# Optimization experiments

Measured on AMD Instinct MI355X. Metric: run time of the kernel, lower is better.

Reference implementation:

```python
import jax, jax.numpy as jnp
import numpy as np

N = 50000      # nodes
E = 800000     # edges (avg degree 16)
IN = 128       # in_channels
OUT = 64       # out_channels
K = 2          # propagation hops


def setup_inputs() -> dict:
    key = jax.random.key(0)
    k1, k2, k3 = jax.random.split(key, 3)
    x = jax.random.normal(k1, (N, IN), dtype=jnp.float32)
    edge_index = jax.random.randint(k2, (2, E), 0, N, dtype=jnp.int32)
    # SGConv's internal Linear(in, out): weight [OUT, IN], bias [OUT]
    W = jax.random.normal(k3, (OUT, IN), dtype=jnp.float32) / np.sqrt(IN)
    b = jnp.zeros((OUT,), dtype=jnp.float32)
    return {"x": x, "edge_index": edge_index, "W": W, "b": b}


def reference(x, edge_index, W, b):
    # GCN normalization with self-loops (PyG gcn_norm, add_self_loops=True)
    row, col = edge_index[0], edge_index[1]
    loops = jnp.arange(N, dtype=edge_index.dtype)
    row = jnp.concatenate([row, loops])   # source nodes
    col = jnp.concatenate([col, loops])   # target nodes
    ones = jnp.ones((E + N,), dtype=x.dtype)
    deg = jax.ops.segment_sum(ones, col, num_segments=N)          # in-degree incl. self-loop
    deg_inv_sqrt = jnp.where(deg > 0, jax.lax.rsqrt(deg), 0.0)
    norm = deg_inv_sqrt[row] * deg_inv_sqrt[col]                  # [E+N]

    # K-hop propagation: x <- D^{-1/2} (A+I) D^{-1/2} x
    for _ in range(K):
        x = jax.ops.segment_sum(x[row] * norm[:, None], col, num_segments=N)

    # final linear; dropout is identity in eval mode (training=False)
    return x @ W.T + b
```

## Files before the change

### kernel.cpp

```cpp
#include <hip/hip_runtime.h>
#include <hip/hip_bf16.h>
#include <hip/hip_fp16.h>

#define IN_CH 128
#define OUT_CH 64
#define NB 512

typedef _Float16 hh2 __attribute__((ext_vector_type(2)));

__global__ void __launch_bounds__(512) histo_kernel(const int* __restrict__ col,
                                                    int* __restrict__ blkcnt,
                                                    int E, int chunk) {
    __shared__ int h[256];
    int blk = blockIdx.x, tid = threadIdx.x;
    if (tid < 256) h[tid] = 0;
    __syncthreads();
    int s = blk * chunk, e = min(s + chunk, E);
    for (int i = s + tid; i < e; i += 512)
        atomicAdd(&h[col[i] >> 8], 1);
    __syncthreads();
    if (tid < 256) blkcnt[blk * 256 + tid] = h[tid];
}

__global__ void __launch_bounds__(256) scanblk_kernel(int* __restrict__ blkcnt,
                                                      int* __restrict__ totals) {
    __shared__ int ps[256];
    int b = blockIdx.x, tid = threadIdx.x;
    int i0 = (2 * tid) * 256 + b, i1 = (2 * tid + 1) * 256 + b;
    int a0 = blkcnt[i0], a1 = blkcnt[i1];
    int lsum = a0 + a1;
    ps[tid] = lsum;
    __syncthreads();
    for (int d = 1; d < 256; d <<= 1) {
        int t = 0;
        if (tid >= d) t = ps[tid - d];
        __syncthreads();
        if (tid >= d) ps[tid] += t;
        __syncthreads();
    }
    int excl = ps[tid] - lsum;
    blkcnt[i0] = excl;
    blkcnt[i1] = excl + a0;
    if (tid == 255) totals[b] = excl + lsum;
}

__global__ void __launch_bounds__(512) bucket_scatter_kernel(const int* __restrict__ row,
                                                             const int* __restrict__ col,
                                                             const int* __restrict__ blkcnt,
                                                             const int* __restrict__ totals,
                                                             unsigned int* __restrict__ tmp,
                                                             int E, int chunk, int nbkt) {
    __shared__ int ps[256];
    __shared__ int cur[256];
    int blk = blockIdx.x, tid = threadIdx.x;
    int v = 0;
    if (tid < 256) { v = (tid < nbkt) ? totals[tid] : 0; ps[tid] = v; }
    __syncthreads();
    for (int d = 1; d < 256; d <<= 1) {
        int t = 0;
        if (tid < 256 && tid >= d) t = ps[tid - d];
        __syncthreads();
        if (tid < 256 && tid >= d) ps[tid] += t;
        __syncthreads();
    }
    if (tid < 256) cur[tid] = (ps[tid] - v) + blkcnt[blk * 256 + tid];
    __syncthreads();
    int s = blk * chunk, e = min(s + chunk, E);
    for (int i = s + tid; i < e; i += 512) {
        int c = col[i], r = row[i];
        int p = atomicAdd(&cur[c >> 8], 1);
        tmp[p] = ((unsigned)(c & 255) << 16) | (unsigned)r;
    }
}

__global__ void __launch_bounds__(512) bucket_sort_kernel(const unsigned int* __restrict__ tmp,
                                                          const int* __restrict__ totals,
                                                          int* __restrict__ off,
                                                          float* __restrict__ dis,
                                                          unsigned short* __restrict__ eidx,
                                                          int nbkt, int E, int n) {
    __shared__ int bs[256];
    __shared__ int cntl[256];
    __shared__ int sc[256];
    __shared__ int posl[256];
    int b = blockIdx.x, tid = threadIdx.x;
    int v = 0;
    if (tid < 256) { v = (tid < nbkt) ? totals[tid] : 0; bs[tid] = v; }
    __syncthreads();
    for (int d = 1; d < 256; d <<= 1) {
        int t = 0;
        if (tid < 256 && tid >= d) t = bs[tid - d];
        __syncthreads();
        if (tid < 256 && tid >= d) bs[tid] += t;
        __syncthreads();
    }
    if (tid < 256) bs[tid] -= v;
    if (tid < 256) cntl[tid] = 0;
    __syncthreads();
    int s = bs[b];
    int e = s + ((b < nbkt) ? totals[b] : 0);
    for (int i = s + tid; i < e; i += 512)
        atomicAdd(&cntl[tmp[i] >> 16], 1);
    __syncthreads();
    int c = 0;
    if (tid < 256) { c = cntl[tid]; sc[tid] = c; }
    __syncthreads();
    for (int d = 1; d < 256; d <<= 1) {
        int t = 0;
        if (tid < 256 && tid >= d) t = sc[tid - d];
        __syncthreads();
        if (tid < 256 && tid >= d) sc[tid] += t;
        __syncthreads();
    }
    if (tid < 256) {
        int excl = sc[tid] - c;
        int gid = (b << 8) + tid;
        if (gid < n) {
            off[gid] = s + excl;
            dis[gid] = rsqrtf((float)(c + 1));
        }
        posl[tid] = s + excl;
    }
    if (b == 0 && tid == 0) off[n] = E;
    __syncthreads();
    for (int i = s + tid; i < e; i += 512) {
        unsigned int w = tmp[i];
        int p = atomicAdd(&posl[w >> 16], 1);
        eidx[p] = (unsigned short)(w & 0xFFFFu);
    }
}

__global__ void __launch_bounds__(256) gemm_kernel(const float* __restrict__ x,
                                                   const float* __restrict__ W,
                                                   const float* __restrict__ dis,
                                                   __half* __restrict__ z, int n) {
    __shared__ hh2 Xs[64 * 66];
    __shared__ hh2 Ws[64 * 66];
    int t = threadIdx.x;
    int m0 = blockIdx.x * 64;
#pragma unroll
    for (int r = 0; r < 8; ++r) {
        int f = t + 256 * r;
        int o = f >> 5, kq = f & 31;
        float4 w = ((const float4*)W)[f];
        Ws[o * 66 + kq * 2]     = hh2{(_Float16)w.x, (_Float16)w.y};
        Ws[o * 66 + kq * 2 + 1] = hh2{(_Float16)w.z, (_Float16)w.w};
    }
#pragma unroll
    for (int r = 0; r < 8; ++r) {
        int f = t + 256 * r;
        int node = f >> 5, kq = f & 31;
        int gv = min(m0 + node, n - 1);
        float4 xv = ((const float4*)(x + (size_t)gv * IN_CH))[kq];
        Xs[node * 66 + kq * 2]     = hh2{(_Float16)xv.x, (_Float16)xv.y};
        Xs[node * 66 + kq * 2 + 1] = hh2{(_Float16)xv.z, (_Float16)xv.w};
    }
    __syncthreads();
    int tx = t & 15, ty = t >> 4;
    float acc[4][4];
#pragma unroll
    for (int i = 0; i < 4; ++i)
#pragma unroll
        for (int j = 0; j < 4; ++j) acc[i][j] = 0.f;

#pragma unroll 4
    for (int kq = 0; kq < 32; ++kq) {
        hh2 xa0[4], xa1[4], wb0[4], wb1[4];
#pragma unroll
        for (int i = 0; i < 4; ++i) {
            int base = (tx + 16 * i) * 66 + kq * 2;
            xa0[i] = Xs[base]; xa1[i] = Xs[base + 1];
        }
#pragma unroll
        for (int j = 0; j < 4; ++j) {
            int base = (ty * 4 + j) * 66 + kq * 2;
            wb0[j] = Ws[base]; wb1[j] = Ws[base + 1];
        }
#pragma unroll
        for (int i = 0; i < 4; ++i)
#pragma unroll
            for (int j = 0; j < 4; ++j) {
                float s = acc[i][j];
                s = __builtin_amdgcn_fdot2(xa0[i], wb0[j], s, false);
                s = __builtin_amdgcn_fdot2(xa1[i], wb1[j], s, false);
                acc[i][j] = s;
            }
    }
#pragma unroll
    for (int i = 0; i < 4; ++i) {
        int v = m0 + tx + 16 * i;
        if (v < n) {
            float dv = dis[v];
            union { __half2 h[2]; float2 f; } u;
            u.h[0] = __floats2half2_rn(dv * acc[i][0], dv * acc[i][1]);
            u.h[1] = __floats2half2_rn(dv * acc[i][2], dv * acc[i][3]);
            *(float2*)&z[(size_t)v * OUT_CH + ty * 4] = u.f;
        }
    }
}

#define ACC8(raw) { const __half2* h2_ = (const __half2*)&(raw);              \
    float2 f0_ = __half22float2(h2_[0]), f1_ = __half22float2(h2_[1]);        \
    float2 f2_ = __half22float2(h2_[2]), f3_ = __half22float2(h2_[3]);        \
    a0 += f0_.x; a1 += f0_.y; a2 += f1_.x; a3 += f1_.y;                       \
    a4 += f2_.x; a5 += f2_.y; a6 += f3_.x; a7 += f3_.y; }

template <int MODE>
__global__ void __launch_bounds__(256) hop_kernel(const __half* __restrict__ zin,
                                                  void* __restrict__ out,
                                                  const unsigned short* __restrict__ eidx,
                                                  const int* __restrict__ off,
                                                  const float* __restrict__ dis,
                                                  const float* __restrict__ bias, int n) {
    int v = (int)((blockIdx.x * 256 + threadIdx.x) >> 6);
    if (v >= n) return;
    int lane = threadIdx.x & 63;
    int grp = lane >> 3;
    int sub = lane & 7;
    int s = off[v], e = off[v + 1];
    float dv = dis[v];
    float a0 = 0.f, a1 = 0.f, a2 = 0.f, a3 = 0.f;
    float a4 = 0.f, a5 = 0.f, a6 = 0.f, a7 = 0.f;
    if (grp == 0) {
        float4 raw = ((const float4*)(zin + (size_t)v * OUT_CH))[sub];
        ACC8(raw);
    }
    int i0 = s + grp;
    int i1 = i0 + 8, i2 = i0 + 16, i3 = i0 + 24;
    bool h0 = i0 < e, h1 = i1 < e, h2 = i2 < e, h3 = i3 < e;
    int r0 = h0 ? (int)eidx[i0] : 0;
    int r1 = h1 ? (int)eidx[i1] : 0;
    int r2 = h2 ? (int)eidx[i2] : 0;
    int r3 = h3 ? (int)eidx[i3] : 0;
    float4 rA = make_float4(0.f, 0.f, 0.f, 0.f);
    float4 rB = make_float4(0.f, 0.f, 0.f, 0.f);
    float4 rC = make_float4(0.f, 0.f, 0.f, 0.f);
    float4 rD = make_float4(0.f, 0.f, 0.f, 0.f);
    if (h0) rA = ((const float4*)(zin + (size_t)r0 * OUT_CH))[sub];
    if (h1) rB = ((const float4*)(zin + (size_t)r1 * OUT_CH))[sub];
    if (h2) rC = ((const float4*)(zin + (size_t)r2 * OUT_CH))[sub];
    if (h3) rD = ((const float4*)(zin + (size_t)r3 * OUT_CH))[sub];
    ACC8(rA); ACC8(rB); ACC8(rC); ACC8(rD);
    if (e - s > 32) {
        int j0 = s + 32 + grp, j1 = j0 + 8;
        bool g0 = j0 < e, g1 = j1 < e;
        int q0 = g0 ? (int)eidx[j0] : 0;
        int q1 = g1 ? (int)eidx[j1] : 0;
        while (g0) {
            int k0 = j0 + 16, k1 = j1 + 16;
            bool f0 = k0 < e, f1 = k1 < e;
            int p0 = f0 ? (int)eidx[k0] : 0;
            int p1 = f1 ? (int)eidx[k1] : 0;
            float4 xA = make_float4(0.f, 0.f, 0.f, 0.f);
            float4 xB = make_float4(0.f, 0.f, 0.f, 0.f);
            if (g0) xA = ((const float4*)(zin + (size_t)q0 * OUT_CH))[sub];
            if (g1) xB = ((const float4*)(zin + (size_t)q1 * OUT_CH))[sub];
            ACC8(xA); ACC8(xB);
            j0 = k0; j1 = k1; q0 = p0; q1 = p1; g0 = f0; g1 = f1;
        }
    }
#pragma unroll
    for (int m = 8; m <= 32; m <<= 1) {
        a0 += __shfl_xor(a0, m, 64); a1 += __shfl_xor(a1, m, 64);
        a2 += __shfl_xor(a2, m, 64); a3 += __shfl_xor(a3, m, 64);
        a4 += __shfl_xor(a4, m, 64); a5 += __shfl_xor(a5, m, 64);
        a6 += __shfl_xor(a6, m, 64); a7 += __shfl_xor(a7, m, 64);
    }
    if (grp == 0) {
        if (MODE == 0) {
            float sc = dv * dv;
            union { __half2 h[4]; float4 f; } u;
            u.h[0] = __floats2half2_rn(sc * a0, sc * a1);
            u.h[1] = __floats2half2_rn(sc * a2, sc * a3);
            u.h[2] = __floats2half2_rn(sc * a4, sc * a5);
            u.h[3] = __floats2half2_rn(sc * a6, sc * a7);
            ((float4*)((__half*)out + (size_t)v * OUT_CH))[sub] = u.f;
        } else {
            const float4* bp = (const float4*)(bias + sub * 8);
            float4 b0 = bp[0], b1 = bp[1];
            float* op = (float*)out + (size_t)v * OUT_CH + sub * 8;
            *(float4*)op = make_float4(fmaf(dv, a0, b0.x), fmaf(dv, a1, b0.y),
                                       fmaf(dv, a2, b0.z), fmaf(dv, a3, b0.w));
            *(float4*)(op + 4) = make_float4(fmaf(dv, a4, b1.x), fmaf(dv, a5, b1.y),
                                             fmaf(dv, a6, b1.z), fmaf(dv, a7, b1.w));
        }
    }
}

extern "C" void kernel_launch(void* const* d_in, const int* in_sizes, int n_in,
                              void* d_out, int out_size, void* d_ws, size_t ws_size,
                              hipStream_t stream) {
    const float* x = (const float*)d_in[0];
    const int* ei = (const int*)d_in[1];
    const float* W = (const float*)d_in[2];
    const float* b = (const float*)d_in[3];
    int n = in_sizes[0] / IN_CH;
    int E = in_sizes[1] / 2;
    const int* row = ei;
    const int* col = ei + E;

    char* ws = (char*)d_ws;
    size_t o = 0;
    auto alloc = [&](size_t bytes) -> void* {
        void* p = ws + o;
        o += (bytes + 255) & ~(size_t)255;
        return p;
    };
    int nbkt = (n + 255) >> 8;
    int chunk = (E + NB - 1) / NB;

    int*            blkcnt = (int*)alloc((size_t)NB * 256 * 4);
    int*            totals = (int*)alloc(256 * 4);
    unsigned int*   tmp    = (unsigned int*)alloc((size_t)E * 4);
    int*            off    = (int*)alloc((size_t)(n + 1) * 4);
    float*          dis    = (float*)alloc((size_t)n * 4);
    unsigned short* eidx   = (unsigned short*)alloc((size_t)E * 2);
    __half*         zA     = (__half*)alloc((size_t)n * OUT_CH * 2);
    __half*         zB     = (__half*)alloc((size_t)n * OUT_CH * 2);

    histo_kernel<<<NB, 512, 0, stream>>>(col, blkcnt, E, chunk);
    scanblk_kernel<<<nbkt, 256, 0, stream>>>(blkcnt, totals);
    bucket_scatter_kernel<<<NB, 512, 0, stream>>>(row, col, blkcnt, totals, tmp, E, chunk, nbkt);
    bucket_sort_kernel<<<nbkt, 512, 0, stream>>>(tmp, totals, off, dis, eidx, nbkt, E, n);
    gemm_kernel<<<(n + 63) / 64, 256, 0, stream>>>(x, W, dis, zA, n);
    int hopBlocks = (n + 3) / 4;
    hop_kernel<0><<<hopBlocks, 256, 0, stream>>>(zA, zB, eidx, off, dis, nullptr, n);
    hop_kernel<1><<<hopBlocks, 256, 0, stream>>>(zB, d_out, eidx, off, dis, b, n);
}
```

Before: 157.6 us.

## Merge preprocessing and compute stages into two cooperative persistent kernels

Replaces seven separate kernel launches with two cooperative kernels that separate the former stages with grid-wide syncs. One kernel covers histogram, scan, bucket scatter and bucket sort. The other runs the GEMM and both propagation hops with grid-stride loops. The aim is to cut per-launch overhead and inter-kernel gaps, at the cost of grid.sync latency and fewer resident blocks for the hop phases. The original multi-kernel path is kept as a fallback if the cooperative launch fails.

```diff
diff --git a/kernel.cpp b/kernel.cpp
--- a/kernel.cpp
+++ b/kernel.cpp
@@ -1,200 +1,132 @@
 #include <hip/hip_runtime.h>
+#include <hip/hip_cooperative_groups.h>
 #include <hip/hip_bf16.h>
 #include <hip/hip_fp16.h>
+
+namespace cg = cooperative_groups;
 
 #define IN_CH 128
 #define OUT_CH 64
 #define NB 512
+#define CB 1024
 
 typedef _Float16 hh2 __attribute__((ext_vector_type(2)));
 
-__global__ void __launch_bounds__(512) histo_kernel(const int* __restrict__ col,
-                                                    int* __restrict__ blkcnt,
-                                                    int E, int chunk) {
-    __shared__ int h[256];
+__global__ void __launch_bounds__(512, 4) pre_kernel(
+    const int* __restrict__ row, const int* __restrict__ col,
+    int* __restrict__ blkcnt, int* __restrict__ totals,
+    unsigned int* __restrict__ tmp, int* __restrict__ off,
+    float* __restrict__ dis, unsigned short* __restrict__ eidx,
+    int E, int n, int chunk, int nbkt)
+{
+    __shared__ int sm[1024];
+    cg::grid_group grid = cg::this_grid();
     int blk = blockIdx.x, tid = threadIdx.x;
-    if (tid < 256) h[tid] = 0;
-    __syncthreads();
-    int s = blk * chunk, e = min(s + chunk, E);
-    for (int i = s + tid; i < e; i += 512)
-        atomicAdd(&h[col[i] >> 8], 1);
-    __syncthreads();
-    if (tid < 256) blkcnt[blk * 256 + tid] = h[tid];
-}
-
-__global__ void __launch_bounds__(256) scanblk_kernel(int* __restrict__ blkcnt,
-                                                      int* __restrict__ totals) {
-    __shared__ int ps[256];
-    int b = blockIdx.x, tid = threadIdx.x;
-    int i0 = (2 * tid) * 256 + b, i1 = (2 * tid + 1) * 256 + b;
-    int a0 = blkcnt[i0], a1 = blkcnt[i1];
-    int lsum = a0 + a1;
-    ps[tid] = lsum;
-    __syncthreads();
-    for (int d = 1; d < 256; d <<= 1) {
-        int t = 0;
-        if (tid >= d) t = ps[tid - d];
-        __syncthreads();
-        if (tid >= d) ps[tid] += t;
-        __syncthreads();
-    }
-    int excl = ps[tid] - lsum;
-    blkcnt[i0] = excl;
-    blkcnt[i1] = excl + a0;
-    if (tid == 255) totals[b] = excl + lsum;
-}
-
-__global__ void __launch_bounds__(512) bucket_scatter_kernel(const int* __restrict__ row,
-                                                             const int* __restrict__ col,
-                                                             const int* __restrict__ blkcnt,
-                                                             const int* __restrict__ totals,
-                                                             unsigned int* __restrict__ tmp,
-                                                             int E, int chunk, int nbkt) {
-    __shared__ int ps[256];
-    __shared__ int cur[256];
-    int blk = blockIdx.x, tid = threadIdx.x;
-    int v = 0;
-    if (tid < 256) { v = (tid < nbkt) ? totals[tid] : 0; ps[tid] = v; }
-    __syncthreads();
-    for (int d = 1; d < 256; d <<= 1) {
-        int t = 0;
-        if (tid < 256 && tid >= d) t = ps[tid - d];
-        __syncthreads();
-        if (tid < 256 && tid >= d) ps[tid] += t;
-        __syncthreads();
-    }
-    if (tid < 256) cur[tid] = (ps[tid] - v) + blkcnt[blk * 256 + tid];
-    __syncthreads();
-    int s = blk * chunk, e = min(s + chunk, E);
-    for (int i = s + tid; i < e; i += 512) {
-        int c = col[i], r = row[i];
-        int p = atomicAdd(&cur[c >> 8], 1);
-        tmp[p] = ((unsigned)(c & 255) << 16) | (unsigned)r;
-    }
-}
-
-__global__ void __launch_bounds__(512) bucket_sort_kernel(const unsigned int* __restrict__ tmp,
-                                                          const int* __restrict__ totals,
-                                                          int* __restrict__ off,
-                                                          float* __restrict__ dis,
-                                                          unsigned short* __restrict__ eidx,
-                                                          int nbkt, int E, int n) {
-    __shared__ int bs[256];
-    __shared__ int cntl[256];
-    __shared__ int sc[256];
-    __shared__ int posl[256];
-    int b = blockIdx.x, tid = threadIdx.x;
-    int v = 0;
-    if (tid < 256) { v = (tid < nbkt) ? totals[tid] : 0; bs[tid] = v; }
-    __syncthreads();
-    for (int d = 1; d < 256; d <<= 1) {
-        int t = 0;
-        if (tid < 256 && tid >= d) t = bs[tid - d];
-        __syncthreads();
-        if (tid < 256 && tid >= d) bs[tid] += t;
-        __syncthreads();
-    }
-    if (tid < 256) bs[tid] -= v;
-    if (tid < 256) cntl[tid] = 0;
-    __syncthreads();
-    int s = bs[b];
-    int e = s + ((b < nbkt) ? totals[b] : 0);
-    for (int i = s + tid; i < e; i += 512)
-        atomicAdd(&cntl[tmp[i] >> 16], 1);
-    __syncthreads();
-    int c = 0;
-    if (tid < 256) { c = cntl[tid]; sc[tid] = c; }
-    __syncthreads();
-    for (int d = 1; d < 256; d <<= 1) {
-        int t = 0;
-        if (tid < 256 && tid >= d) t = sc[tid - d];
-        __syncthreads();
-        if (tid < 256 && tid >= d) sc[tid] += t;
-        __syncthreads();
-    }
-    if (tid < 256) {
-        int excl = sc[tid] - c;
-        int gid = (b << 8) + tid;
-        if (gid < n) {
-            off[gid] = s + excl;
-            dis[gid] = rsqrtf((float)(c + 1));
-        }
-        posl[tid] = s + excl;
-    }
-    if (b == 0 && tid == 0) off[n] = E;
-    __syncthreads();
-    for (int i = s + tid; i < e; i += 512) {
-        unsigned int w = tmp[i];
-        int p = atomicAdd(&posl[w >> 16], 1);
-        eidx[p] = (unsigned short)(w & 0xFFFFu);
-    }
-}
-
-__global__ void __launch_bounds__(256) gemm_kernel(const float* __restrict__ x,
-                                                   const float* __restrict__ W,
-                                                   const float* __restrict__ dis,
-                                                   __half* __restrict__ z, int n) {
-    __shared__ hh2 Xs[64 * 66];
-    __shared__ hh2 Ws[64 * 66];
-    int t = threadIdx.x;
-    int m0 = blockIdx.x * 64;
-#pragma unroll
-    for (int r = 0; r < 8; ++r) {
-        int f = t + 256 * r;
-        int o = f >> 5, kq = f & 31;
-        float4 w = ((const float4*)W)[f];
-        Ws[o * 66 + kq * 2]     = hh2{(_Float16)w.x, (_Float16)w.y};
-        Ws[o * 66 + kq * 2 + 1] = hh2{(_Float16)w.z, (_Float16)w.w};
-    }
-#pragma unroll
-    for (int r = 0; r < 8; ++r) {
-        int f = t + 256 * r;
-        int node = f >> 5, kq = f & 31;
-        int gv = min(m0 + node, n - 1);
-        float4 xv = ((const float4*)(x + (size_t)gv * IN_CH))[kq];
-        Xs[node * 66 + kq * 2]     = hh2{(_Float16)xv.x, (_Float16)xv.y};
-        Xs[node * 66 + kq * 2 + 1] = hh2{(_Float16)xv.z, (_Float16)xv.w};
-    }
-    __syncthreads();
-    int tx = t & 15, ty = t >> 4;
-    float acc[4][4];
-#pragma unroll
-    for (int i = 0; i < 4; ++i)
-#pragma unroll
-        for (int j = 0; j < 4; ++j) acc[i][j] = 0.f;
-
-#pragma unroll 4
-    for (int kq = 0; kq < 32; ++kq) {
-        hh2 xa0[4], xa1[4], wb0[4], wb1[4];
-#pragma unroll
-        for (int i = 0; i < 4; ++i) {
-            int base = (tx + 16 * i) * 66 + kq * 2;
-            xa0[i] = Xs[base]; xa1[i] = Xs[base + 1];
-        }
-#pragma unroll
-        for (int j = 0; j < 4; ++j) {
-            int base = (ty * 4 + j) * 66 + kq * 2;
-            wb0[j] = Ws[base]; wb1[j] = Ws[base + 1];
-        }
-#pragma unroll
-        for (int i = 0; i < 4; ++i)
-#pragma unroll
-            for (int j = 0; j < 4; ++j) {
-                float s = acc[i][j];
-                s = __builtin_amdgcn_fdot2(xa0[i], wb0[j], s, false);
-                s = __builtin_amdgcn_fdot2(xa1[i], wb1[j], s, false);
-                acc[i][j] = s;
+
+    if (tid < 256) sm[tid] = 0;
+    __syncthreads();
+    {
+        int s = blk * chunk, e = min(s + chunk, E);
+        for (int i = s + tid; i < e; i += 512)
+            atomicAdd(&sm[col[i] >> 8], 1);
+    }
+    __syncthreads();
+    if (tid < 256) blkcnt[blk * 256 + tid] = sm[tid];
+    grid.sync();
+
+    if (blk < nbkt) {
+        int i0 = 0, i1 = 0, a0 = 0, a1 = 0, lsum = 0;
+        if (tid < 256) {
+            i0 = (2 * tid) * 256 + blk; i1 = (2 * tid + 1) * 256 + blk;
+            a0 = blkcnt[i0]; a1 = blkcnt[i1];
+            lsum = a0 + a1;
+            sm[tid] = lsum;
+        }
+        __syncthreads();
+        for (int d = 1; d < 256; d <<= 1) {
+            int t = 0;
+            if (tid < 256 && tid >= d) t = sm[tid - d];
+            __syncthreads();
+            if (tid < 256 && tid >= d) sm[tid] += t;
+            __syncthreads();
+        }
+        if (tid < 256) {
+            int excl = sm[tid] - lsum;
+            blkcnt[i0] = excl;
+            blkcnt[i1] = excl + a0;
+            if (tid == 255) totals[blk] = excl + lsum;
+        }
+    }
+    grid.sync();
+
+    {
+        int* ps = sm; int* cur = sm + 256;
+        int v = 0;
+        if (tid < 256) { v = (tid < nbkt) ? totals[tid] : 0; ps[tid] = v; }
+        __syncthreads();
+        for (int d = 1; d < 256; d <<= 1) {
+            int t = 0;
+            if (tid < 256 && tid >= d) t = ps[tid - d];
+            __syncthreads();
+            if (tid < 256 && tid >= d) ps[tid] += t;
+            __syncthreads();
+        }
+        if (tid < 256) cur[tid] = (ps[tid] - v) + blkcnt[blk * 256 + tid];
+        __syncthreads();
+        int s = blk * chunk, e = min(s + chunk, E);
+        for (int i = s + tid; i < e; i += 512) {
+            int c = col[i], r = row[i];
+            int p = atomicAdd(&cur[c >> 8], 1);
+            tmp[p] = ((unsigned)(c & 255) << 16) | (unsigned)r;
+        }
+    }
+    grid.sync();
+
+    if (blk < nbkt) {
+        int* bs = sm; int* cntl = sm + 256; int* sc = sm + 512; int* posl = sm + 768;
+        int v = 0;
+        if (tid < 256) { v = (tid < nbkt) ? totals[tid] : 0; bs[tid] = v; }
+        __syncthreads();
+        for (int d = 1; d < 256; d <<= 1) {
+            int t = 0;
+            if (tid < 256 && tid >= d) t = bs[tid - d];
+            __syncthreads();
+            if (tid < 256 && tid >= d) bs[tid] += t;
+            __syncthreads();
+        }
+        if (tid < 256) bs[tid] -= v;
+        if (tid < 256) cntl[tid] = 0;
+        __syncthreads();
+        int s = bs[blk];
+        int e = s + totals[blk];
+        for (int i = s + tid; i < e; i += 512)
+            atomicAdd(&cntl[tmp[i] >> 16], 1);
+        __syncthreads();
+        int c = 0;
+        if (tid < 256) { c = cntl[tid]; sc[tid] = c; }
+        __syncthreads();
+        for (int d = 1; d < 256; d <<= 1) {
+            int t = 0;
+            if (tid < 256 && tid >= d) t = sc[tid - d];
+            __syncthreads();
+            if (tid < 256 && tid >= d) sc[tid] += t;
+            __syncthreads();
+        }
+        if (tid < 256) {
+            int excl = sc[tid] - c;
+            int gid = (blk << 8) + tid;
+            if (gid < n) {
+                off[gid] = s + excl;
+                dis[gid] = rsqrtf((float)(c + 1));
             }
-    }
-#pragma unroll
-    for (int i = 0; i < 4; ++i) {
-        int v = m0 + tx + 16 * i;
-        if (v < n) {
-            float dv = dis[v];
-            union { __half2 h[2]; float2 f; } u;
-            u.h[0] = __floats2half2_rn(dv * acc[i][0], dv * acc[i][1]);
-            u.h[1] = __floats2half2_rn(dv * acc[i][2], dv * acc[i][3]);
-            *(float2*)&z[(size_t)v * OUT_CH + ty * 4] = u.f;
+            posl[tid] = s + excl;
+        }
+        if (blk == 0 && tid == 0) off[n] = E;
+        __syncthreads();
+        for (int i = s + tid; i < e; i += 512) {
+            unsigned int w = tmp[i];
+            int p = atomicAdd(&posl[w >> 16], 1);
+            eidx[p] = (unsigned short)(w & 0xFFFFu);
         }
     }
 }
@@ -206,15 +138,14 @@
     a4 += f2_.x; a5 += f2_.y; a6 += f3_.x; a7 += f3_.y; }
 
 template <int MODE>
-__global__ void __launch_bounds__(256) hop_kernel(const __half* __restrict__ zin,
-                                                  void* __restrict__ out,
-                                                  const unsigned short* __restrict__ eidx,
-                                                  const int* __restrict__ off,
-                                                  const float* __restrict__ dis,
-                                                  const float* __restrict__ bias, int n) {
-    int v = (int)((blockIdx.x * 256 + threadIdx.x) >> 6);
-    if (v >= n) return;
-    int lane = threadIdx.x & 63;
+__device__ __forceinline__ void hop_node(int v, int lane,
+                                         const __half* __restrict__ zin,
+                                         void* __restrict__ out,
+                                         const unsigned short* __restrict__ eidx,
+                                         const int* __restrict__ off,
+                                         const float* __restrict__ dis,
+                                         const float* __restrict__ bias)
+{
     int grp = lane >> 3;
     int sub = lane & 7;
     int s = off[v], e = off[v + 1];
@@ -287,6 +218,297 @@
     }
 }
 
+__global__ void __launch_bounds__(256, 4) compute_kernel(
+    const float* __restrict__ x, const float* __restrict__ W,
+    const float* __restrict__ dis, const float* __restrict__ bias,
+    __half* __restrict__ zA, __half* __restrict__ zB,
+    float* __restrict__ outF,
+    const unsigned short* __restrict__ eidx, const int* __restrict__ off,
+    int n)
+{
+    __shared__ hh2 Xs[64 * 66];
+    __shared__ hh2 Ws[64 * 66];
+    cg::grid_group grid = cg::this_grid();
+    int t = threadIdx.x;
+
+    int ntiles = (n + 63) >> 6;
+    for (int tile = blockIdx.x; tile < ntiles; tile += gridDim.x) {
+        int m0 = tile * 64;
+#pragma unroll
+        for (int r = 0; r < 8; ++r) {
+            int f = t + 256 * r;
+            int o = f >> 5, kq = f & 31;
+            float4 w = ((const float4*)W)[f];
+            Ws[o * 66 + kq * 2]     = hh2{(_Float16)w.x, (_Float16)w.y};
+            Ws[o * 66 + kq * 2 + 1] = hh2{(_Float16)w.z, (_Float16)w.w};
+        }
+#pragma unroll
+        for (int r = 0; r < 8; ++r) {
+            int f = t + 256 * r;
+            int node = f >> 5, kq = f & 31;
+            int gv = min(m0 + node, n - 1);
+            float4 xv = ((const float4*)(x + (size_t)gv * IN_CH))[kq];
+            Xs[node * 66 + kq * 2]     = hh2{(_Float16)xv.x, (_Float16)xv.y};
+            Xs[node * 66 + kq * 2 + 1] = hh2{(_Float16)xv.z, (_Float16)xv.w};
+        }
+        __syncthreads();
+        int tx = t & 15, ty = t >> 4;
+        float acc[4][4];
+#pragma unroll
+        for (int i = 0; i < 4; ++i)
+#pragma unroll
+            for (int j = 0; j < 4; ++j) acc[i][j] = 0.f;
+#pragma unroll 4
+        for (int kq = 0; kq < 32; ++kq) {
+            hh2 xa0[4], xa1[4], wb0[4], wb1[4];
+#pragma unroll
+            for (int i = 0; i < 4; ++i) {
+                int base = (tx + 16 * i) * 66 + kq * 2;
+                xa0[i] = Xs[base]; xa1[i] = Xs[base + 1];
+            }
+#pragma unroll
+            for (int j = 0; j < 4; ++j) {
+                int base = (ty * 4 + j) * 66 + kq * 2;
+                wb0[j] = Ws[base]; wb1[j] = Ws[base + 1];
+            }
+#pragma unroll
+            for (int i = 0; i < 4; ++i)
+#pragma unroll
+                for (int j = 0; j < 4; ++j) {
+                    float s = acc[i][j];
+                    s = __builtin_amdgcn_fdot2(xa0[i], wb0[j], s, false);
+                    s = __builtin_amdgcn_fdot2(xa1[i], wb1[j], s, false);
+                    acc[i][j] = s;
+                }
+        }
+#pragma unroll
+        for (int i = 0; i < 4; ++i) {
+            int v = m0 + tx + 16 * i;
+            if (v < n) {
+                float dv = dis[v];
+                union { __half2 h[2]; float2 f; } u;
+                u.h[0] = __floats2half2_rn(dv * acc[i][0], dv * acc[i][1]);
+                u.h[1] = __floats2half2_rn(dv * acc[i][2], dv * acc[i][3]);
+                *(float2*)&zA[(size_t)v * OUT_CH + ty * 4] = u.f;
+            }
+        }
+        __syncthreads();
+    }
+    grid.sync();
+
+    int waveId = (int)((blockIdx.x * 256 + t) >> 6);
+    int nwaves = (int)((gridDim.x * 256) >> 6);
+    int lane = t & 63;
+    for (int v = waveId; v < n; v += nwaves)
+        hop_node<0>(v, lane, zA, (void*)zB, eidx, off, dis, nullptr);
+    grid.sync();
+
+    for (int v = waveId; v < n; v += nwaves)
+        hop_node<1>(v, lane, zB, (void*)outF, eidx, off, dis, bias);
+}
+
+__global__ void __launch_bounds__(512) histo_kernel(const int* __restrict__ col,
+                                                    int* __restrict__ blkcnt,
+                                                    int E, int chunk) {
+    __shared__ int h[256];
+    int blk = blockIdx.x, tid = threadIdx.x;
+    if (tid < 256) h[tid] = 0;
+    __syncthreads();
+    int s = blk * chunk, e = min(s + chunk, E);
+    for (int i = s + tid; i < e; i += 512)
+        atomicAdd(&h[col[i] >> 8], 1);
+    __syncthreads();
+    if (tid < 256) blkcnt[blk * 256 + tid] = h[tid];
+}
+
+__global__ void __launch_bounds__(256) scanblk_kernel(int* __restrict__ blkcnt,
+                                                      int* __restrict__ totals) {
+    __shared__ int ps[256];
+    int b = blockIdx.x, tid = threadIdx.x;
+    int i0 = (2 * tid) * 256 + b, i1 = (2 * tid + 1) * 256 + b;
+    int a0 = blkcnt[i0], a1 = blkcnt[i1];
+    int lsum = a0 + a1;
+    ps[tid] = lsum;
+    __syncthreads();
+    for (int d = 1; d < 256; d <<= 1) {
+        int t = 0;
+        if (tid >= d) t = ps[tid - d];
+        __syncthreads();
+        if (tid >= d) ps[tid] += t;
+        __syncthreads();
+    }
+    int excl = ps[tid] - lsum;
+    blkcnt[i0] = excl;
+    blkcnt[i1] = excl + a0;
+    if (tid == 255) totals[b] = excl + lsum;
+}
+
+__global__ void __launch_bounds__(512) bucket_scatter_kernel(const int* __restrict__ row,
+                                                             const int* __restrict__ col,
+                                                             const int* __restrict__ blkcnt,
+                                                             const int* __restrict__ totals,
+                                                             unsigned int* __restrict__ tmp,
+                                                             int E, int chunk, int nbkt) {
+    __shared__ int ps[256];
+    __shared__ int cur[256];
+    int blk = blockIdx.x, tid = threadIdx.x;
+    int v = 0;
+    if (tid < 256) { v = (tid < nbkt) ? totals[tid] : 0; ps[tid] = v; }
+    __syncthreads();
+    for (int d = 1; d < 256; d <<= 1) {
+        int t = 0;
+        if (tid < 256 && tid >= d) t = ps[tid - d];
+        __syncthreads();
+        if (tid < 256 && tid >= d) ps[tid] += t;
+        __syncthreads();
+    }
+    if (tid < 256) cur[tid] = (ps[tid] - v) + blkcnt[blk * 256 + tid];
+    __syncthreads();
+    int s = blk * chunk, e = min(s + chunk, E);
+    for (int i = s + tid; i < e; i += 512) {
+        int c = col[i], r = row[i];
+        int p = atomicAdd(&cur[c >> 8], 1);
+        tmp[p] = ((unsigned)(c & 255) << 16) | (unsigned)r;
+    }
+}
+
+__global__ void __launch_bounds__(512) bucket_sort_kernel(const unsigned int* __restrict__ tmp,
+                                                          const int* __restrict__ totals,
+                                                          int* __restrict__ off,
+                                                          float* __restrict__ dis,
+                                                          unsigned short* __restrict__ eidx,
+                                                          int nbkt, int E, int n) {
+    __shared__ int bs[256];
+    __shared__ int cntl[256];
+    __shared__ int sc[256];
+    __shared__ int posl[256];
+    int b = blockIdx.x, tid = threadIdx.x;
+    int v = 0;
+    if (tid < 256) { v = (tid < nbkt) ? totals[tid] : 0; bs[tid] = v; }
+    __syncthreads();
+    for (int d = 1; d < 256; d <<= 1) {
+        int t = 0;
+        if (tid < 256 && tid >= d) t = bs[tid - d];
+        __syncthreads();
+        if (tid < 256 && tid >= d) bs[tid] += t;
+        __syncthreads();
+    }
+    if (tid < 256) bs[tid] -= v;
+    if (tid < 256) cntl[tid] = 0;
+    __syncthreads();
+    int s = bs[b];
+    int e = s + ((b < nbkt) ? totals[b] : 0);
+    for (int i = s + tid; i < e; i += 512)
+        atomicAdd(&cntl[tmp[i] >> 16], 1);
+    __syncthreads();
+    int c = 0;
+    if (tid < 256) { c = cntl[tid]; sc[tid] = c; }
+    __syncthreads();
+    for (int d = 1; d < 256; d <<= 1) {
+        int t = 0;
+        if (tid < 256 && tid >= d) t = sc[tid - d];
+        __syncthreads();
+        if (tid < 256 && tid >= d) sc[tid] += t;
+        __syncthreads();
+    }
+    if (tid < 256) {
+        int excl = sc[tid] - c;
+        int gid = (b << 8) + tid;
+        if (gid < n) {
+            off[gid] = s + excl;
+            dis[gid] = rsqrtf((float)(c + 1));
+        }
+        posl[tid] = s + excl;
+    }
+    if (b == 0 && tid == 0) off[n] = E;
+    __syncthreads();
+    for (int i = s + tid; i < e; i += 512) {
+        unsigned int w = tmp[i];
+        int p = atomicAdd(&posl[w >> 16], 1);
+        eidx[p] = (unsigned short)(w & 0xFFFFu);
+    }
+}
+
+__global__ void __launch_bounds__(256) gemm_kernel(const float* __restrict__ x,
+                                                   const float* __restrict__ W,
+                                                   const float* __restrict__ dis,
+                                                   __half* __restrict__ z, int n) {
+    __shared__ hh2 Xs[64 * 66];
+    __shared__ hh2 Ws[64 * 66];
+    int t = threadIdx.x;
+    int m0 = blockIdx.x * 64;
+#pragma unroll
+    for (int r = 0; r < 8; ++r) {
+        int f = t + 256 * r;
+        int o = f >> 5, kq = f & 31;
+        float4 w = ((const float4*)W)[f];
+        Ws[o * 66 + kq * 2]     = hh2{(_Float16)w.x, (_Float16)w.y};
+        Ws[o * 66 + kq * 2 + 1] = hh2{(_Float16)w.z, (_Float16)w.w};
+    }
+#pragma unroll
+    for (int r = 0; r < 8; ++r) {
+        int f = t + 256 * r;
+        int node = f >> 5, kq = f & 31;
+        int gv = min(m0 + node, n - 1);
+        float4 xv = ((const float4*)(x + (size_t)gv * IN_CH))[kq];
+        Xs[node * 66 + kq * 2]     = hh2{(_Float16)xv.x, (_Float16)xv.y};
+        Xs[node * 66 + kq * 2 + 1] = hh2{(_Float16)xv.z, (_Float16)xv.w};
+    }
+    __syncthreads();
+    int tx = t & 15, ty = t >> 4;
+    float acc[4][4];
+#pragma unroll
+    for (int i = 0; i < 4; ++i)
+#pragma unroll
+        for (int j = 0; j < 4; ++j) acc[i][j] = 0.f;
+#pragma unroll 4
+    for (int kq = 0; kq < 32; ++kq) {
+        hh2 xa0[4], xa1[4], wb0[4], wb1[4];
+#pragma unroll
+        for (int i = 0; i < 4; ++i) {
+            int base = (tx + 16 * i) * 66 + kq * 2;
+            xa0[i] = Xs[base]; xa1[i] = Xs[base + 1];
+        }
+#pragma unroll
+        for (int j = 0; j < 4; ++j) {
+            int base = (ty * 4 + j) * 66 + kq * 2;
+            wb0[j] = Ws[base]; wb1[j] = Ws[base + 1];
+        }
+#pragma unroll
+        for (int i = 0; i < 4; ++i)
+#pragma unroll
+            for (int j = 0; j < 4; ++j) {
+                float s = acc[i][j];
+                s = __builtin_amdgcn_fdot2(xa0[i], wb0[j], s, false);
+                s = __builtin_amdgcn_fdot2(xa1[i], wb1[j], s, false);
+                acc[i][j] = s;
+            }
+    }
+#pragma unroll
+    for (int i = 0; i < 4; ++i) {
+        int v = m0 + tx + 16 * i;
+        if (v < n) {
+            float dv = dis[v];
+            union { __half2 h[2]; float2 f; } u;
+            u.h[0] = __floats2half2_rn(dv * acc[i][0], dv * acc[i][1]);
+            u.h[1] = __floats2half2_rn(dv * acc[i][2], dv * acc[i][3]);
+            *(float2*)&z[(size_t)v * OUT_CH + ty * 4] = u.f;
+        }
+    }
+}
+
+template <int MODE>
+__global__ void __launch_bounds__(256) hop_kernel(const __half* __restrict__ zin,
+                                                  void* __restrict__ out,
+                                                  const unsigned short* __restrict__ eidx,
+                                                  const int* __restrict__ off,
+                                                  const float* __restrict__ dis,
+                                                  const float* __restrict__ bias, int n) {
+    int v = (int)((blockIdx.x * 256 + threadIdx.x) >> 6);
+    if (v >= n) return;
+    hop_node<MODE>(v, threadIdx.x & 63, zin, out, eidx, off, dis, bias);
+}
+
 extern "C" void kernel_launch(void* const* d_in, const int* in_sizes, int n_in,
                               void* d_out, int out_size, void* d_ws, size_t ws_size,
                               hipStream_t stream) {
@@ -317,13 +539,35 @@
     unsigned short* eidx   = (unsigned short*)alloc((size_t)E * 2);
     __half*         zA     = (__half*)alloc((size_t)n * OUT_CH * 2);
     __half*         zB     = (__half*)alloc((size_t)n * OUT_CH * 2);
-
-    histo_kernel<<<NB, 512, 0, stream>>>(col, blkcnt, E, chunk);
-    scanblk_kernel<<<nbkt, 256, 0, stream>>>(blkcnt, totals);
-    bucket_scatter_kernel<<<NB, 512, 0, stream>>>(row, col, blkcnt, totals, tmp, E, chunk, nbkt);
-    bucket_sort_kernel<<<nbkt, 512, 0, stream>>>(tmp, totals, off, dis, eidx, nbkt, E, n);
-    gemm_kernel<<<(n + 63) / 64, 256, 0, stream>>>(x, W, dis, zA, n);
-    int hopBlocks = (n + 3) / 4;
-    hop_kernel<0><<<hopBlocks, 256, 0, stream>>>(zA, zB, eidx, off, dis, nullptr, n);
-    hop_kernel<1><<<hopBlocks, 256, 0, stream>>>(zB, d_out, eidx, off, dis, b, n);
-}
+    float*          outF   = (float*)d_out;
+
+    {
+        void* pargs[] = {(void*)&row, (void*)&col, (void*)&blkcnt, (void*)&totals,
+                         (void*)&tmp, (void*)&off, (void*)&dis, (void*)&eidx,
+                         (void*)&E, (void*)&n, (void*)&chunk, (void*)&nbkt};
+        hipError_t err = hipLaunchCooperativeKernel((const void*)pre_kernel,
+                                                    dim3(NB), dim3(512), pargs, 0, stream);
+        if (err != hipSuccess) {
+            (void)hipGetLastError();
+            histo_kernel<<<NB, 512, 0, stream>>>(col, blkcnt, E, chunk);
+            scanblk_kernel<<<nbkt, 256, 0, stream>>>(blkcnt, totals);
+            bucket_scatter_kernel<<<NB, 512, 0, stream>>>(row, col, blkcnt, totals, tmp, E, chunk, nbkt);
+            bucket_sort_kernel<<<nbkt, 512, 0, stream>>>(tmp, totals, off, dis, eidx, nbkt, E, n);
+        }
+    }
+
+    {
+        void* cargs[] = {(void*)&x, (void*)&W, (void*)&dis, (void*)&b,
+                         (void*)&zA, (void*)&zB, (void*)&outF,
+                         (void*)&eidx, (void*)&off, (void*)&n};
+        hipError_t err = hipLaunchCooperativeKernel((const void*)compute_kernel,
+                                                    dim3(CB), dim3(256), cargs, 0, stream);
+        if (err != hipSuccess) {
+            (void)hipGetLastError();
+            gemm_kernel<<<(n + 63) / 64, 256, 0, stream>>>(x, W, dis, zA, n);
+            int hopBlocks = (n + 3) / 4;
+            hop_kernel<0><<<hopBlocks, 256, 0, stream>>>(zA, (void*)zB, eidx, off, dis, nullptr, n);
+            hop_kernel<1><<<hopBlocks, 256, 0, stream>>>(zB, (void*)outF, eidx, off, dis, b, n);
+        }
+    }
+}
```

Measured after the change: 587.0 us. +272.6%, slower.

## Stage bucket scatter and sort outputs in shared memory for coalesced global writes

Applied to the files above, without the earlier changes.

Scatter now groups each block's chunk by bucket in LDS, records destinations, then writes tmp in bucket-contiguous runs. Sort likewise assembles each bucket's eidx in LDS before a linear copy, replacing random 2-byte global stores. Block count drops from 512 to 256 so chunks fit the LDS cap, with a raw-count buffer added for local offsets. This aims to cut scattered global writes in preprocessing, at the cost of more LDS use and fewer blocks.

```diff
diff --git a/kernel.cpp b/kernel.cpp
--- a/kernel.cpp
+++ b/kernel.cpp
@@ -4,12 +4,15 @@
 
 #define IN_CH 128
 #define OUT_CH 64
-#define NB 512
+#define NB 256
+#define CHUNK_CAP 3200
+#define SORT_CAP 6144
 
 typedef _Float16 hh2 __attribute__((ext_vector_type(2)));
 
 __global__ void __launch_bounds__(512) histo_kernel(const int* __restrict__ col,
                                                     int* __restrict__ blkcnt,
+                                                    int* __restrict__ rawcnt,
                                                     int E, int chunk) {
     __shared__ int h[256];
     int blk = blockIdx.x, tid = threadIdx.x;
@@ -19,17 +22,19 @@
     for (int i = s + tid; i < e; i += 512)
         atomicAdd(&h[col[i] >> 8], 1);
     __syncthreads();
-    if (tid < 256) blkcnt[blk * 256 + tid] = h[tid];
+    if (tid < 256) {
+        blkcnt[blk * 256 + tid] = h[tid];
+        rawcnt[blk * 256 + tid] = h[tid];
+    }
 }
 
 __global__ void __launch_bounds__(256) scanblk_kernel(int* __restrict__ blkcnt,
                                                       int* __restrict__ totals) {
     __shared__ int ps[256];
     int b = blockIdx.x, tid = threadIdx.x;
-    int i0 = (2 * tid) * 256 + b, i1 = (2 * tid + 1) * 256 + b;
-    int a0 = blkcnt[i0], a1 = blkcnt[i1];
-    int lsum = a0 + a1;
-    ps[tid] = lsum;
+    int i0 = tid * 256 + b;
+    int a0 = blkcnt[i0];
+    ps[tid] = a0;
     __syncthreads();
     for (int d = 1; d < 256; d <<= 1) {
         int t = 0;
@@ -38,38 +43,66 @@
         if (tid >= d) ps[tid] += t;
         __syncthreads();
     }
-    int excl = ps[tid] - lsum;
-    blkcnt[i0] = excl;
-    blkcnt[i1] = excl + a0;
-    if (tid == 255) totals[b] = excl + lsum;
+    blkcnt[i0] = ps[tid] - a0;
+    if (tid == 255) totals[b] = ps[255];
 }
 
 __global__ void __launch_bounds__(512) bucket_scatter_kernel(const int* __restrict__ row,
                                                              const int* __restrict__ col,
                                                              const int* __restrict__ blkcnt,
+                                                             const int* __restrict__ rawcnt,
                                                              const int* __restrict__ totals,
                                                              unsigned int* __restrict__ tmp,
                                                              int E, int chunk, int nbkt) {
     __shared__ int ps[256];
-    __shared__ int cur[256];
+    __shared__ int ls[256];
+    __shared__ int bias[256];
+    __shared__ int curl[256];
+    __shared__ unsigned int vall[CHUNK_CAP];
+    __shared__ int destl[CHUNK_CAP];
     int blk = blockIdx.x, tid = threadIdx.x;
-    int v = 0;
-    if (tid < 256) { v = (tid < nbkt) ? totals[tid] : 0; ps[tid] = v; }
+    int t0 = 0, lr = 0;
+    if (tid < 256) {
+        t0 = (tid < nbkt) ? totals[tid] : 0;
+        ps[tid] = t0;
+        lr = rawcnt[blk * 256 + tid];
+        ls[tid] = lr;
+    }
     __syncthreads();
     for (int d = 1; d < 256; d <<= 1) {
-        int t = 0;
-        if (tid < 256 && tid >= d) t = ps[tid - d];
-        __syncthreads();
-        if (tid < 256 && tid >= d) ps[tid] += t;
-        __syncthreads();
-    }
-    if (tid < 256) cur[tid] = (ps[tid] - v) + blkcnt[blk * 256 + tid];
+        int t = 0, u = 0;
+        if (tid < 256 && tid >= d) { t = ps[tid - d]; u = ls[tid - d]; }
+        __syncthreads();
+        if (tid < 256 && tid >= d) { ps[tid] += t; ls[tid] += u; }
+        __syncthreads();
+    }
+    if (tid < 256) {
+        int bucket_base = ps[tid] - t0;
+        int loff = ls[tid] - lr;
+        bias[tid] = bucket_base + blkcnt[blk * 256 + tid] - loff;
+        curl[tid] = loff;
+    }
     __syncthreads();
     int s = blk * chunk, e = min(s + chunk, E);
-    for (int i = s + tid; i < e; i += 512) {
-        int c = col[i], r = row[i];
-        int p = atomicAdd(&cur[c >> 8], 1);
-        tmp[p] = ((unsigned)(c & 255) << 16) | (unsigned)r;
+    int csize = e - s;
+    if (csize <= CHUNK_CAP) {
+        for (int i = s + tid; i < e; i += 512) {
+            int c = col[i], r = row[i];
+            int k = c >> 8;
+            int p = atomicAdd(&curl[k], 1);
+            vall[p]  = ((unsigned)(c & 255) << 16) | (unsigned)r;
+            destl[p] = bias[k] + p;
+        }
+        __syncthreads();
+        for (int j = tid; j < csize; j += 512)
+            tmp[destl[j]] = vall[j];
+    } else {
+        for (int i = s + tid; i < e; i += 512) {
+            int c = col[i], r = row[i];
+            int k = c >> 8;
+            int p = atomicAdd(&curl[k], 1);
+            tmp[bias[k] + p] = ((unsigned)(c & 255) << 16) | (unsigned)r;
+        }
     }
 }
 
@@ -82,7 +115,8 @@
     __shared__ int bs[256];
     __shared__ int cntl[256];
     __shared__ int sc[256];
-    __shared__ int posl[256];
+    __shared__ int posr[256];
+    __shared__ unsigned short el[SORT_CAP];
     int b = blockIdx.x, tid = threadIdx.x;
     int v = 0;
     if (tid < 256) { v = (tid < nbkt) ? totals[tid] : 0; bs[tid] = v; }
@@ -98,7 +132,8 @@
     if (tid < 256) cntl[tid] = 0;
     __syncthreads();
     int s = bs[b];
-    int e = s + ((b < nbkt) ? totals[b] : 0);
+    int cnt = (b < nbkt) ? totals[b] : 0;
+    int e = s + cnt;
     for (int i = s + tid; i < e; i += 512)
         atomicAdd(&cntl[tmp[i] >> 16], 1);
     __syncthreads();
@@ -119,14 +154,26 @@
             off[gid] = s + excl;
             dis[gid] = rsqrtf((float)(c + 1));
         }
-        posl[tid] = s + excl;
+        posr[tid] = excl;
     }
     if (b == 0 && tid == 0) off[n] = E;
     __syncthreads();
-    for (int i = s + tid; i < e; i += 512) {
-        unsigned int w = tmp[i];
-        int p = atomicAdd(&posl[w >> 16], 1);
-        eidx[p] = (unsigned short)(w & 0xFFFFu);
+    bool staged = (cnt <= SORT_CAP);
+    if (staged) {
+        for (int i = s + tid; i < e; i += 512) {
+            unsigned int w = tmp[i];
+            int p = atomicAdd(&posr[w >> 16], 1);
+            el[p] = (unsigned short)(w & 0xFFFFu);
+        }
+        __syncthreads();
+        for (int i = tid; i < cnt; i += 512)
+            eidx[s + i] = el[i];
+    } else {
+        for (int i = s + tid; i < e; i += 512) {
+            unsigned int w = tmp[i];
+            int p = atomicAdd(&posr[w >> 16], 1);
+            eidx[s + p] = (unsigned short)(w & 0xFFFFu);
+        }
     }
 }
 
@@ -310,6 +357,7 @@
     int chunk = (E + NB - 1) / NB;
 
     int*            blkcnt = (int*)alloc((size_t)NB * 256 * 4);
+    int*            rawcnt = (int*)alloc((size_t)NB * 256 * 4);
     int*            totals = (int*)alloc(256 * 4);
     unsigned int*   tmp    = (unsigned int*)alloc((size_t)E * 4);
     int*            off    = (int*)alloc((size_t)(n + 1) * 4);
@@ -318,9 +366,9 @@
     __half*         zA     = (__half*)alloc((size_t)n * OUT_CH * 2);
     __half*         zB     = (__half*)alloc((size_t)n * OUT_CH * 2);
 
-    histo_kernel<<<NB, 512, 0, stream>>>(col, blkcnt, E, chunk);
+    histo_kernel<<<NB, 512, 0, stream>>>(col, blkcnt, rawcnt, E, chunk);
     scanblk_kernel<<<nbkt, 256, 0, stream>>>(blkcnt, totals);
-    bucket_scatter_kernel<<<NB, 512, 0, stream>>>(row, col, blkcnt, totals, tmp, E, chunk, nbkt);
+    bucket_scatter_kernel<<<NB, 512, 0, stream>>>(row, col, blkcnt, rawcnt, totals, tmp, E, chunk, nbkt);
     bucket_sort_kernel<<<nbkt, 512, 0, stream>>>(tmp, totals, off, dis, eidx, nbkt, E, n);
     gemm_kernel<<<(n + 63) / 64, 256, 0, stream>>>(x, W, dis, zA, n);
     int hopBlocks = (n + 3) / 4;
```

New measurement: 153.7 us. -2.4%, faster.

## Replace bucket-sort CSR build with atomic degree count fused into GEMM

Applied to the files above, without the earlier changes.

Drops the four-kernel two-level bucket sort (histogram, block scan, bucket scatter, in-bucket sort). In its place, in-degrees are counted with global atomics in extra blocks of the GEMM launch. A prep kernel then computes offsets by block reduction and scan, writes the normalization factors, and converts the fp32 GEMM output to scaled fp16. A final kernel scatters edges by per-node atomic cursors. This cuts launches and the intermediate packed buffer, but adds an fp32 z0 round trip and redundant prefix sums per block. Neighbor order within a node also becomes nondeterministic.

```diff
diff --git a/kernel.cpp b/kernel.cpp
--- a/kernel.cpp
+++ b/kernel.cpp
@@ -4,139 +4,28 @@
 
 #define IN_CH 128
 #define OUT_CH 64
-#define NB 512
+#define HB 256
 
 typedef _Float16 hh2 __attribute__((ext_vector_type(2)));
 
-__global__ void __launch_bounds__(512) histo_kernel(const int* __restrict__ col,
-                                                    int* __restrict__ blkcnt,
-                                                    int E, int chunk) {
-    __shared__ int h[256];
-    int blk = blockIdx.x, tid = threadIdx.x;
-    if (tid < 256) h[tid] = 0;
-    __syncthreads();
-    int s = blk * chunk, e = min(s + chunk, E);
-    for (int i = s + tid; i < e; i += 512)
-        atomicAdd(&h[col[i] >> 8], 1);
-    __syncthreads();
-    if (tid < 256) blkcnt[blk * 256 + tid] = h[tid];
-}
-
-__global__ void __launch_bounds__(256) scanblk_kernel(int* __restrict__ blkcnt,
-                                                      int* __restrict__ totals) {
-    __shared__ int ps[256];
-    int b = blockIdx.x, tid = threadIdx.x;
-    int i0 = (2 * tid) * 256 + b, i1 = (2 * tid + 1) * 256 + b;
-    int a0 = blkcnt[i0], a1 = blkcnt[i1];
-    int lsum = a0 + a1;
-    ps[tid] = lsum;
-    __syncthreads();
-    for (int d = 1; d < 256; d <<= 1) {
-        int t = 0;
-        if (tid >= d) t = ps[tid - d];
-        __syncthreads();
-        if (tid >= d) ps[tid] += t;
-        __syncthreads();
-    }
-    int excl = ps[tid] - lsum;
-    blkcnt[i0] = excl;
-    blkcnt[i1] = excl + a0;
-    if (tid == 255) totals[b] = excl + lsum;
-}
-
-__global__ void __launch_bounds__(512) bucket_scatter_kernel(const int* __restrict__ row,
-                                                             const int* __restrict__ col,
-                                                             const int* __restrict__ blkcnt,
-                                                             const int* __restrict__ totals,
-                                                             unsigned int* __restrict__ tmp,
-                                                             int E, int chunk, int nbkt) {
-    __shared__ int ps[256];
-    __shared__ int cur[256];
-    int blk = blockIdx.x, tid = threadIdx.x;
-    int v = 0;
-    if (tid < 256) { v = (tid < nbkt) ? totals[tid] : 0; ps[tid] = v; }
-    __syncthreads();
-    for (int d = 1; d < 256; d <<= 1) {
-        int t = 0;
-        if (tid < 256 && tid >= d) t = ps[tid - d];
-        __syncthreads();
-        if (tid < 256 && tid >= d) ps[tid] += t;
-        __syncthreads();
-    }
-    if (tid < 256) cur[tid] = (ps[tid] - v) + blkcnt[blk * 256 + tid];
-    __syncthreads();
-    int s = blk * chunk, e = min(s + chunk, E);
-    for (int i = s + tid; i < e; i += 512) {
-        int c = col[i], r = row[i];
-        int p = atomicAdd(&cur[c >> 8], 1);
-        tmp[p] = ((unsigned)(c & 255) << 16) | (unsigned)r;
-    }
-}
-
-__global__ void __launch_bounds__(512) bucket_sort_kernel(const unsigned int* __restrict__ tmp,
-                                                          const int* __restrict__ totals,
-                                                          int* __restrict__ off,
-                                                          float* __restrict__ dis,
-                                                          unsigned short* __restrict__ eidx,
-                                                          int nbkt, int E, int n) {
-    __shared__ int bs[256];
-    __shared__ int cntl[256];
-    __shared__ int sc[256];
-    __shared__ int posl[256];
-    int b = blockIdx.x, tid = threadIdx.x;
-    int v = 0;
-    if (tid < 256) { v = (tid < nbkt) ? totals[tid] : 0; bs[tid] = v; }
-    __syncthreads();
-    for (int d = 1; d < 256; d <<= 1) {
-        int t = 0;
-        if (tid < 256 && tid >= d) t = bs[tid - d];
-        __syncthreads();
-        if (tid < 256 && tid >= d) bs[tid] += t;
-        __syncthreads();
-    }
-    if (tid < 256) bs[tid] -= v;
-    if (tid < 256) cntl[tid] = 0;
-    __syncthreads();
-    int s = bs[b];
-    int e = s + ((b < nbkt) ? totals[b] : 0);
-    for (int i = s + tid; i < e; i += 512)
-        atomicAdd(&cntl[tmp[i] >> 16], 1);
-    __syncthreads();
-    int c = 0;
-    if (tid < 256) { c = cntl[tid]; sc[tid] = c; }
-    __syncthreads();
-    for (int d = 1; d < 256; d <<= 1) {
-        int t = 0;
-        if (tid < 256 && tid >= d) t = sc[tid - d];
-        __syncthreads();
-        if (tid < 256 && tid >= d) sc[tid] += t;
-        __syncthreads();
-    }
-    if (tid < 256) {
-        int excl = sc[tid] - c;
-        int gid = (b << 8) + tid;
-        if (gid < n) {
-            off[gid] = s + excl;
-            dis[gid] = rsqrtf((float)(c + 1));
-        }
-        posl[tid] = s + excl;
-    }
-    if (b == 0 && tid == 0) off[n] = E;
-    __syncthreads();
-    for (int i = s + tid; i < e; i += 512) {
-        unsigned int w = tmp[i];
-        int p = atomicAdd(&posl[w >> 16], 1);
-        eidx[p] = (unsigned short)(w & 0xFFFFu);
-    }
-}
-
-__global__ void __launch_bounds__(256) gemm_kernel(const float* __restrict__ x,
-                                                   const float* __restrict__ W,
-                                                   const float* __restrict__ dis,
-                                                   __half* __restrict__ z, int n) {
+__global__ void __launch_bounds__(256) fat_kernel(const float* __restrict__ x,
+                                                  const float* __restrict__ W,
+                                                  float* __restrict__ z0,
+                                                  const int* __restrict__ col,
+                                                  int* __restrict__ deg,
+                                                  int n, int E, int GB) {
     __shared__ hh2 Xs[64 * 66];
     __shared__ hh2 Ws[64 * 66];
     int t = threadIdx.x;
+
+    if (blockIdx.x >= GB) {
+        int i = (blockIdx.x - GB) * 256 + t;
+        int step = HB * 256;
+        for (; i < E; i += step)
+            atomicAdd(&deg[col[i]], 1);
+        return;
+    }
+
     int m0 = blockIdx.x * 64;
 #pragma unroll
     for (int r = 0; r < 8; ++r) {
@@ -189,13 +78,90 @@
 #pragma unroll
     for (int i = 0; i < 4; ++i) {
         int v = m0 + tx + 16 * i;
+        if (v < n)
+            *(float4*)&z0[(size_t)v * OUT_CH + ty * 4] =
+                make_float4(acc[i][0], acc[i][1], acc[i][2], acc[i][3]);
+    }
+}
+
+__global__ void __launch_bounds__(256) prep_kernel(const int* __restrict__ deg,
+                                                   const float* __restrict__ z0,
+                                                   int* __restrict__ off,
+                                                   int* __restrict__ cur,
+                                                   float* __restrict__ dis,
+                                                   __half* __restrict__ zA,
+                                                   int n, int E) {
+    __shared__ int sm[256];
+    __shared__ float dl[256];
+    __shared__ int base_s;
+    int b = blockIdx.x, t = threadIdx.x;
+
+    int s_ = 0;
+    const int4* deg4 = (const int4*)deg;
+    int n4 = b * 64;
+    for (int i = t; i < n4; i += 256) {
+        int4 v = deg4[i];
+        s_ += v.x + v.y + v.z + v.w;
+    }
+    sm[t] = s_;
+    __syncthreads();
+    for (int d = 128; d > 0; d >>= 1) {
+        if (t < d) sm[t] += sm[t + d];
+        __syncthreads();
+    }
+    if (t == 0) base_s = sm[0];
+    __syncthreads();
+    int base = base_s;
+    __syncthreads();
+
+    int v0 = b * 256 + t;
+    int d0 = (v0 < n) ? deg[v0] : 0;
+    sm[t] = d0;
+    __syncthreads();
+    for (int d = 1; d < 256; d <<= 1) {
+        int tv = 0;
+        if (t >= d) tv = sm[t - d];
+        __syncthreads();
+        if (t >= d) sm[t] += tv;
+        __syncthreads();
+    }
+    int excl = sm[t] - d0;
+    float dv = rsqrtf((float)(d0 + 1));
+    if (v0 < n) {
+        off[v0] = base + excl;
+        cur[v0] = base + excl;
+        dis[v0] = dv;
+    }
+    dl[t] = dv;
+    if (b == 0 && t == 0) off[n] = E;
+    __syncthreads();
+
+    const float4* z04 = (const float4*)z0;
+    for (int f = t; f < 256 * 16; f += 256) {
+        int r = f >> 4, c = f & 15;
+        int v = b * 256 + r;
         if (v < n) {
-            float dv = dis[v];
-            union { __half2 h[2]; float2 f; } u;
-            u.h[0] = __floats2half2_rn(dv * acc[i][0], dv * acc[i][1]);
-            u.h[1] = __floats2half2_rn(dv * acc[i][2], dv * acc[i][3]);
-            *(float2*)&z[(size_t)v * OUT_CH + ty * 4] = u.f;
-        }
+            float4 zz = z04[(size_t)v * 16 + c];
+            float s = dl[r];
+            union { __half2 h[2]; float2 fo; } u;
+            u.h[0] = __floats2half2_rn(s * zz.x, s * zz.y);
+            u.h[1] = __floats2half2_rn(s * zz.z, s * zz.w);
+            *(float2*)&zA[(size_t)v * OUT_CH + c * 4] = u.fo;
+        }
+    }
+}
+
+__global__ void __launch_bounds__(256) scatter_kernel(const int* __restrict__ row,
+                                                      const int* __restrict__ col,
+                                                      int* __restrict__ cur,
+                                                      unsigned short* __restrict__ eidx,
+                                                      int E) {
+    int i = blockIdx.x * 256 + threadIdx.x;
+    int step = gridDim.x * 256;
+    for (; i < E; i += step) {
+        int c = col[i], r = row[i];
+        int p = atomicAdd(&cur[c], 1);
+        eidx[p] = (unsigned short)r;
     }
 }
 
@@ -307,22 +273,21 @@
         return p;
     };
     int nbkt = (n + 255) >> 8;
-    int chunk = (E + NB - 1) / NB;
-
-    int*            blkcnt = (int*)alloc((size_t)NB * 256 * 4);
-    int*            totals = (int*)alloc(256 * 4);
-    unsigned int*   tmp    = (unsigned int*)alloc((size_t)E * 4);
-    int*            off    = (int*)alloc((size_t)(n + 1) * 4);
-    float*          dis    = (float*)alloc((size_t)n * 4);
-    unsigned short* eidx   = (unsigned short*)alloc((size_t)E * 2);
-    __half*         zA     = (__half*)alloc((size_t)n * OUT_CH * 2);
-    __half*         zB     = (__half*)alloc((size_t)n * OUT_CH * 2);
-
-    histo_kernel<<<NB, 512, 0, stream>>>(col, blkcnt, E, chunk);
-    scanblk_kernel<<<nbkt, 256, 0, stream>>>(blkcnt, totals);
-    bucket_scatter_kernel<<<NB, 512, 0, stream>>>(row, col, blkcnt, totals, tmp, E, chunk, nbkt);
-    bucket_sort_kernel<<<nbkt, 512, 0, stream>>>(tmp, totals, off, dis, eidx, nbkt, E, n);
-    gemm_kernel<<<(n + 63) / 64, 256, 0, stream>>>(x, W, dis, zA, n);
+    int GB = (n + 63) / 64;
+
+    int*            deg  = (int*)alloc(((size_t)n + 4) * 4);
+    int*            off  = (int*)alloc((size_t)(n + 1) * 4);
+    int*            cur  = (int*)alloc((size_t)n * 4);
+    float*          dis  = (float*)alloc((size_t)n * 4);
+    unsigned short* eidx = (unsigned short*)alloc((size_t)E * 2);
+    float*          z0   = (float*)alloc((size_t)n * OUT_CH * 4);
+    __half*         zA   = (__half*)alloc((size_t)n * OUT_CH * 2);
+    __half*         zB   = (__half*)alloc((size_t)n * OUT_CH * 2);
+
+    hipMemsetAsync(deg, 0, (size_t)n * 4, stream);
+    fat_kernel<<<GB + HB, 256, 0, stream>>>(x, W, z0, col, deg, n, E, GB);
+    prep_kernel<<<nbkt, 256, 0, stream>>>(deg, z0, off, cur, dis, zA, n, E);
+    scatter_kernel<<<1024, 256, 0, stream>>>(row, col, cur, eidx, E);
     int hopBlocks = (n + 3) / 4;
     hop_kernel<0><<<hopBlocks, 256, 0, stream>>>(zA, zB, eidx, off, dis, nullptr, n);
     hop_kernel<1><<<hopBlocks, 256, 0, stream>>>(zB, d_out, eidx, off, dis, b, n);
```

After: 219.0 us. 1.39x slower.
